# Kernel optimization log

Measured on AMD Instinct MI355X. Metric: run time of the kernel, lower is better.

Reference implementation:

```python
import jax, jax.numpy as jnp
import numpy as np
from jax.ops import segment_sum

N = 50000        # nodes
E = 800000       # edges
IN = 128         # in_channels
HID = 128        # hidden_channels
G = 256          # number of graphs


def setup_inputs() -> dict:
    key = jax.random.key(0)
    ks = jax.random.split(key, 24)

    def w(k, shape, fan_in):
        return (jax.random.normal(k, shape, dtype=jnp.float32) / np.sqrt(fan_in)).astype(jnp.float32)

    x = jax.random.normal(ks[0], (N, IN), dtype=jnp.float32)
    pos = jax.random.normal(ks[1], (N, 3), dtype=jnp.float32)
    edge_index = jax.random.randint(ks[2], (2, E), 0, N, dtype=jnp.int64)
    batch = jnp.sort(jax.random.randint(ks[3], (N,), 0, G, dtype=jnp.int64))

    params = dict(
        gcn_w=w(ks[4], (IN, HID), IN), gcn_b=jnp.zeros((HID,), jnp.float32),
        pam_w=w(ks[5], (IN, HID), IN), pam_b=jnp.zeros((HID,), jnp.float32),
        pm_w1=w(ks[6], (3, HID), 3), pm_b1=jnp.zeros((HID,), jnp.float32),
        pm_w2=w(ks[7], (HID, HID), HID), pm_b2=jnp.zeros((HID,), jnp.float32),
        att_w=w(ks[8], (2 * HID, 1), 2 * HID), att_b=jnp.zeros((1,), jnp.float32),
        fus_w=w(ks[9], (2 * HID, HID), 2 * HID), fus_b=jnp.zeros((HID,), jnp.float32),
        l1_w=w(ks[10], (HID, HID // 2), HID), l1_b=jnp.zeros((HID // 2,), jnp.float32),
        l2_w=w(ks[11], (HID // 2, 1), HID // 2), l2_b=jnp.zeros((1,), jnp.float32),
    )
    return dict(x=x, pos=pos, edge_index=edge_index, batch=batch, **params)


def reference(x, pos, edge_index, batch,
              gcn_w, gcn_b, pam_w, pam_b,
              pm_w1, pm_b1, pm_w2, pm_b2,
              att_w, att_b, fus_w, fus_b,
              l1_w, l1_b, l2_w, l2_b):
    n = x.shape[0]
    src, dst = edge_index[0], edge_index[1]  # j = source, i = target (PyG flow)

    # ---- global branch: GCNConv (self-loops + symmetric normalization) ----
    xw = x @ gcn_w                                   # [N, HID]
    loop = jnp.arange(n, dtype=src.dtype)
    s = jnp.concatenate([src, loop])
    d = jnp.concatenate([dst, loop])
    deg = segment_sum(jnp.ones_like(d, dtype=xw.dtype), d, num_segments=n)
    dinv = jnp.where(deg > 0, deg ** -0.5, 0.0)
    norm = dinv[s] * dinv[d]                          # [E+N]
    gcn = segment_sum(norm[:, None] * xw[s], d, num_segments=n) + gcn_b
    global_feat = jax.nn.relu(gcn)

    # ---- local branch: PAMConv ----
    xl = x @ pam_w + pam_b                            # [N, HID]
    x_i, x_j = xl[dst], xl[src]                       # [E, HID]
    delta = pos[dst] - pos[src]                       # [E, 3]
    de = jax.nn.relu(delta @ pm_w1 + pm_b1) @ pm_w2 + pm_b2   # [E, HID]
    att = jax.nn.sigmoid(jnp.concatenate([x_i, x_j], axis=-1) @ att_w + att_b)  # [E,1]
    msg = att * (x_j + de)
    local_feat = jax.nn.relu(segment_sum(msg, dst, num_segments=n))

    # ---- fusion + global mean pool + readout ----
    fused = jax.nn.relu(jnp.concatenate([global_feat, local_feat], axis=-1) @ fus_w + fus_b)
    counts = segment_sum(jnp.ones((n,), fused.dtype), batch, num_segments=G)
    pooled = segment_sum(fused, batch, num_segments=G) / jnp.clip(counts, 1.0)[:, None]
    h = jax.nn.relu(pooled @ l1_w + l1_b)
    return h @ l2_w + l2_b                            # [G, 1]
```

## Files before the change

kernel.cpp:

```cpp
#include <hip/hip_runtime.h>
#include <hip/hip_fp16.h>
#include <math.h>

#define NN 50000
#define NE 800000
#define HD 128
#define NG 256
#define SCAN_B 196
#define NODE_B 12500
#define HIST_B 3125
#define GEM_B 782
#define ZQ2 8192
#define WP_HIST0 73

typedef unsigned int u32;
typedef unsigned short u16;
typedef __attribute__((ext_vector_type(8))) short bf16x8;
typedef __attribute__((ext_vector_type(4))) float f32x4;
typedef __attribute__((ext_vector_type(2))) float f32x2;

__device__ __forceinline__ float wave_allsum(float v) {
#pragma unroll
  for (int m = 1; m < 64; m <<= 1) v += __shfl_xor(v, m, 64);
  return v;
}
__device__ __forceinline__ float bcastf(float v, int t) {
  return __int_as_float(__builtin_amdgcn_readlane(__float_as_int(v), t));
}
__device__ __forceinline__ u32 f2b_bits(float f) {
  u32 u = __float_as_uint(f);
  return (u + 0x7fffu + ((u >> 16) & 1u)) >> 16;
}
__device__ __forceinline__ u32 cvtpk_bf16(float lo, float hi) {
  u32 r;
  asm("v_cvt_pk_bf16_f32 %0, %1, %2" : "=v"(r) : "v"(lo), "v"(hi));
  return r;
}
__device__ __forceinline__ f32x2 splat2(float v) { return (f32x2){v, v}; }
__device__ __forceinline__ f32x2 pkfma(f32x2 a, f32x2 b, f32x2 c) {
  return a * b + c;
}

__global__ __launch_bounds__(256) void k_wpack(
    const float* __restrict__ gcn_w, const float* __restrict__ pam_w,
    const float* __restrict__ pm_w2, const float* __restrict__ fus_w,
    const float* __restrict__ pam_b, const float* __restrict__ att_w,
    const float* __restrict__ att_b, const float* __restrict__ pm_b2,
    u16* __restrict__ Bg, u16* __restrict__ Bl, u16* __restrict__ Bf,
    float* __restrict__ vi, float* __restrict__ vj,
    float* __restrict__ consts, float* __restrict__ bsumv,
    uint4* __restrict__ zr2, const int* __restrict__ ei,
    int* __restrict__ cnt, u16* __restrict__ slot16) {
  if (blockIdx.x >= WP_HIST0) {
    const int e = (blockIdx.x - WP_HIST0) * 256 + threadIdx.x;
    if (e < NE) slot16[e] = (u16)atomicAdd(&cnt[ei[NE + e]], 1);
    return;
  }
  if (blockIdx.x >= 41) {
    const int zi = (blockIdx.x - 41) * 256 + threadIdx.x;
    if (zi < ZQ2) zr2[zi] = (uint4){0u, 0u, 0u, 0u};
    return;
  }
  if (blockIdx.x == 40) {
    const int t = threadIdx.x;
    const int k = t & 127;
    const float* w = att_w + (t >> 7) * HD;
    float s = 0.f;
    for (int h = 0; h < HD; ++h) s = fmaf(pam_w[k * HD + h], w[h], s);
    if (t < 128) {
      vi[k] = s;
      bsumv[k] = pam_b[k] + pm_b2[k];
    } else {
      vj[k] = s;
    }
    if (t < 64) {
      float p = fmaf(pam_b[t], att_w[t], pam_b[t + 64] * att_w[t + 64]);
      p = wave_allsum(p);
      if (t == 0) consts[0] = p + att_b[0];
    } else if (t < 128) {
      const int l = t - 64;
      float p =
          fmaf(pam_b[l], att_w[HD + l], pam_b[l + 64] * att_w[HD + 64 + l]);
      p = wave_allsum(p);
      if (l == 0) consts[1] = p;
    }
    return;
  }
  const int t = blockIdx.x * 256 + threadIdx.x;
  const float* W;
  u16* dst;
  if (t < 2048) {
    const int kb = t >> 7, n = t & 127;
    W = gcn_w + (size_t)kb * 8 * HD + n;
    dst = Bg + (size_t)t * 8;
  } else if (t < 6144) {
    const int u = t - 2048;
    const int kb = u >> 7, n = u & 127;
    W = ((kb < 16) ? (pam_w + (size_t)kb * 8 * HD)
                   : (pm_w2 + (size_t)(kb - 16) * 8 * HD)) +
        n;
    dst = Bl + (size_t)u * 8;
  } else {
    const int u = t - 6144;
    const int kb = u >> 7, n = u & 127;
    W = fus_w + (size_t)kb * 8 * HD + n;
    dst = Bf + (size_t)u * 8;
  }
  union {
    u16 o[8];
    uint4 v;
  } pk;
#pragma unroll
  for (int i = 0; i < 8; ++i) pk.o[i] = (u16)f2b_bits(W[i * HD]);
  *(uint4*)dst = pk.v;
}

__global__ __launch_bounds__(256) void k_scan1(const int* __restrict__ cnt,
                                               int* __restrict__ bsum) {
  const int i = blockIdx.x * 256 + threadIdx.x;
  int v = (i < NN) ? cnt[i] : 0;
#pragma unroll
  for (int m = 1; m < 64; m <<= 1) v += __shfl_xor(v, m, 64);
  __shared__ int s[4];
  if ((threadIdx.x & 63) == 0) s[threadIdx.x >> 6] = v;
  __syncthreads();
  if (threadIdx.x == 0) bsum[blockIdx.x] = s[0] + s[1] + s[2] + s[3];
}

__global__ __launch_bounds__(256) void k_scan23(
    const int* __restrict__ cnt, const int* __restrict__ bsum,
    const float* __restrict__ pos, int* __restrict__ offs,
    float* __restrict__ dinv, float4* __restrict__ posadj) {
  __shared__ int s[256];
  const int t = threadIdx.x;
  const int bv = (t < SCAN_B) ? bsum[t] : 0;
  s[t] = bv;
  __syncthreads();
  for (int d = 1; d < 256; d <<= 1) {
    int add = (t >= d) ? s[t - d] : 0;
    __syncthreads();
    s[t] += add;
    __syncthreads();
  }
  const int bpre = (blockIdx.x > 0) ? s[blockIdx.x - 1] : 0;
  __syncthreads();
  const int i = blockIdx.x * 256 + t;
  const int v = (i < NN) ? cnt[i] : 0;
  s[t] = v;
  __syncthreads();
  for (int d = 1; d < 256; d <<= 1) {
    int add = (t >= d) ? s[t - d] : 0;
    __syncthreads();
    s[t] += add;
    __syncthreads();
  }
  if (i < NN) {
    offs[i] = bpre + s[t] - v;
    dinv[i] = __builtin_amdgcn_rsqf((float)v + 1.0f);
    posadj[i] = make_float4(pos[3 * i], pos[3 * i + 1], pos[3 * i + 2], 0.f);
  }
}

__global__ __launch_bounds__(256) void k_scatgc(
    const int* __restrict__ ei, const int* __restrict__ offs,
    const u16* __restrict__ slot16, int* __restrict__ csr_src,
    const int* __restrict__ batch, float* __restrict__ counts,
    const float* __restrict__ x, const float* __restrict__ dinv,
    const int* __restrict__ cnt, const float* __restrict__ vi,
    const float* __restrict__ vj, const float* __restrict__ consts,
    u16* __restrict__ xq, float* __restrict__ ai_arr,
    float4* __restrict__ posadj) {
  if (blockIdx.x < HIST_B) {
    const int e = blockIdx.x * 256 + threadIdx.x;
    if (e < NE) {
      const int d = ei[NE + e];
      csr_src[offs[d] + slot16[e]] = ei[e];
    }
    return;
  }
  if (blockIdx.x == HIST_B) {
    const int g = threadIdx.x;
    int lo = 0, hi = NN;
    while (lo < hi) {
      const int mid = (lo + hi) >> 1;
      if (batch[mid] < g) lo = mid + 1; else hi = mid;
    }
    const int b0 = lo;
    hi = NN;
    while (lo < hi) {
      const int mid = (lo + hi) >> 1;
      if (batch[mid] <= g) lo = mid + 1; else hi = mid;
    }
    counts[g] = (float)(lo - b0);
    return;
  }
  const int wave = threadIdx.x >> 6, lane = threadIdx.x & 63;
  const int i = (blockIdx.x - HIST_B - 1) * 4 + wave;
  if (i >= NN) return;
  const float2 v = *(const float2*)&x[(size_t)i * HD + lane * 2];
  const float dv = dinv[i];
  const u32 q = __builtin_amdgcn_cvt_pk_fp8_f32(dv * v.x, dv * v.y, 0u, false);
  xq[(size_t)i * 64 + lane] = (u16)q;
  const float2 a = *(const float2*)&vi[lane * 2];
  const float2 b = *(const float2*)&vj[lane * 2];
  float si = wave_allsum(fmaf(v.x, a.x, v.y * a.y));
  float sj = wave_allsum(fmaf(v.x, b.x, v.y * b.y));
  if (lane == 0) {
    ai_arr[i] = si + consts[0];
    const u32 wb =
        (u32)__half_as_ushort(__float2half(sj + consts[1])) |
        ((u32)__half_as_ushort(__float2half(sqrtf((float)cnt[i] + 1.f)))
         << 16);
    ((float*)(posadj + i))[3] = __uint_as_float(wb);
  }
}

__global__ __launch_bounds__(256) void k_agg(
    const u16* __restrict__ xq, const float4* __restrict__ posadj,
    const int* __restrict__ csr_src, const int* __restrict__ offs,
    const int* __restrict__ cnt, const float* __restrict__ ai_arr,
    const float* __restrict__ pm_w1, const float* __restrict__ pm_b1,
    u32* __restrict__ ZG, u32* __restrict__ XT, float* __restrict__ sa_out) {
  const int wave = threadIdx.x >> 6, lane = threadIdx.x & 63;
  const int i = blockIdx.x * 4 + wave;
  if (i >= NN) return;
  const int c0 = lane * 2;

  const f32x2 w1x = *(const f32x2*)&pm_w1[c0];
  const f32x2 w1y = *(const f32x2*)&pm_w1[HD + c0];
  const f32x2 w1z = *(const f32x2*)&pm_w1[2 * HD + c0];
  const f32x2 b1 = *(const f32x2*)&pm_b1[c0];
  const float ai = ai_arr[i];
  const float4 pi = posadj[i];

  f32x2 zg = {0.f, 0.f}, xa = {0.f, 0.f}, tt = {0.f, 0.f};
  float sa = 0.f;
  const int b = offs[i], e = b + cnt[i];
  for (int base = b; base < e; base += 64) {
    const int mm = min(64, e - base);
    const int sk = csr_src[base + ((lane < mm) ? lane : 0)];
    const float4 pa = posadj[sk];
    const u32 wb = __float_as_uint(pa.w);
    const float aj = __half2float(__ushort_as_half((u16)(wb & 0xffffu)));
    const float sdeg = __half2float(__ushort_as_half((u16)(wb >> 16)));
    float attk = __builtin_amdgcn_rcpf(1.f + __expf(-(ai + aj)));
    const float apk = attk * sdeg;
    const float dxk = pi.x - pa.x;
    const float dyk = pi.y - pa.y;
    const float dzk = pi.z - pa.z;
    if (lane >= mm) attk = 0.f;
    sa += wave_allsum(attk);

    for (int s16 = 0; s16 < mm; s16 += 16) {
      const int n16 = min(16, mm - s16);
      u32 rr[16];
#pragma unroll
      for (int u = 0; u < 16; ++u) {
        if (u < n16) {
          const int s = __builtin_amdgcn_readlane(sk, s16 + u);
          rr[u] = *(xq + ((size_t)s << 6) + lane);
        }
      }
#pragma unroll
      for (int u = 0; u < 16; ++u) {
        if (u < n16) {
          const int T = s16 + u;
          const float att = bcastf(attk, T);
          const float ap = bcastf(apk, T);
          const float dx = bcastf(dxk, T);
          const float dy = bcastf(dyk, T);
          const float dz = bcastf(dzk, T);
          const f32x2 y = __builtin_amdgcn_cvt_pk_f32_fp8(rr[u], false);
          zg += y;
          xa = pkfma(splat2(ap), y, xa);
          f32x2 gg = pkfma(splat2(dz), w1z,
                           pkfma(splat2(dy), w1y,
                                 pkfma(splat2(dx), w1x, b1)));
          gg = __builtin_elementwise_max(gg, splat2(0.f));
          tt = pkfma(splat2(att), gg, tt);
        }
      }
    }
  }
  const u32 xi = *(xq + ((size_t)i << 6) + lane);
  zg += __builtin_amdgcn_cvt_pk_f32_fp8(xi, false);

  ZG[(size_t)i * 64 + lane] = cvtpk_bf16(zg.x, zg.y);
  XT[(size_t)i * 128 + lane] = cvtpk_bf16(xa.x, xa.y);
  XT[(size_t)i * 128 + 64 + lane] = cvtpk_bf16(tt.x, tt.y);
  if (lane == 0) sa_out[i] = sa;
}

template <int K16>
__device__ __forceinline__ void phase_g2(const u16* __restrict__ pa,
                                         const u16* __restrict__ pb0,
                                         f32x4 acc[8]) {
  bf16x8 a[3], b[3][8];
#pragma unroll
  for (int p = 0; p < 2; ++p) {
    a[p] = *(const bf16x8*)(pa + p * 32);
    const u16* pn = pb0 + (size_t)p * 4096;
#pragma unroll
    for (int cf = 0; cf < 8; ++cf) b[p][cf] = *(const bf16x8*)(pn + cf * 128);
  }
#pragma unroll
  for (int k0 = 0; k0 < K16; ++k0) {
    if (k0 + 2 < K16) {
      const int nb = (k0 + 2) % 3;
      a[nb] = *(const bf16x8*)(pa + (k0 + 2) * 32);
      const u16* pn = pb0 + (size_t)(k0 + 2) * 4096;
#pragma unroll
      for (int cf = 0; cf < 8; ++cf)
        b[nb][cf] = *(const bf16x8*)(pn + cf * 128);
    }
    const int cb = k0 % 3;
#pragma unroll
    for (int cf = 0; cf < 8; ++cf)
      acc[cf] = __builtin_amdgcn_mfma_f32_16x16x32_bf16(a[cb], b[cb][cf],
                                                        acc[cf], 0, 0, 0);
  }
}

__global__ __launch_bounds__(256, 3) void k_gemms(
    const u16* __restrict__ ZG, const u16* __restrict__ XT,
    const u16* __restrict__ Bg, const u16* __restrict__ Bl,
    const u16* __restrict__ Bf, const float* __restrict__ dinv,
    const float* __restrict__ sa, const float* __restrict__ gcn_b,
    const float* __restrict__ bsumv, const float* __restrict__ fus_b,
    const int* __restrict__ batch, float* __restrict__ pooled) {
  __shared__ u16 T[64 * 256];
  __shared__ int batch_lds[64];
  const int n0 = blockIdx.x * 64;
  const int t = threadIdx.x, lane = t & 63, w = t >> 6;
  const int m = lane & 15, g = lane >> 4;
  const int r0 = w * 16;

  if (t < 64) batch_lds[t] = (n0 + t < NN) ? batch[n0 + t] : -1;

  const int rowA = min(n0 + r0 + m, NN - 1);
  f32x4 acc[8];

#pragma unroll
  for (int cf = 0; cf < 8; ++cf) acc[cf] = (f32x4){0.f, 0.f, 0.f, 0.f};
  phase_g2<4>(ZG + (size_t)rowA * 128 + g * 8, Bg + ((size_t)g * HD + m) * 8,
              acc);
#pragma unroll
  for (int j = 0; j < 4; ++j) {
    const int rl = r0 + g * 4 + j;
    const float dv = dinv[min(n0 + rl, NN - 1)];
#pragma unroll
    for (int cf = 0; cf < 8; ++cf) {
      const float v = fmaxf(fmaf(dv, acc[cf][j], gcn_b[cf * 16 + m]), 0.f);
      T[rl * 256 + ((cf * 16 + m) ^ ((rl & 7) << 3))] = (u16)f2b_bits(v);
    }
  }

#pragma unroll
  for (int cf = 0; cf < 8; ++cf) acc[cf] = (f32x4){0.f, 0.f, 0.f, 0.f};
  phase_g2<8>(XT + (size_t)rowA * 256 + g * 8, Bl + ((size_t)g * HD + m) * 8,
              acc);
#pragma unroll
  for (int j = 0; j < 4; ++j) {
    const int rl = r0 + g * 4 + j;
    const float sv = sa[min(n0 + rl, NN - 1)];
#pragma unroll
    for (int cf = 0; cf < 8; ++cf) {
      const float v = fmaxf(fmaf(sv, bsumv[cf * 16 + m], acc[cf][j]), 0.f);
      T[rl * 256 + ((128 + cf * 16 + m) ^ ((rl & 7) << 3))] = (u16)f2b_bits(v);
    }
  }

  const int x0m = (m & 7) << 3;
  const u16* rowT = &T[(r0 + m) * 256];
  const u16* pbC = Bf + ((size_t)g * HD + m) * 8;
#pragma unroll
  for (int cf = 0; cf < 8; ++cf) acc[cf] = (f32x4){0.f, 0.f, 0.f, 0.f};
  {
    bf16x8 a[3], b[3][8];
#pragma unroll
    for (int p = 0; p < 2; ++p) {
      a[p] = *(const bf16x8*)&rowT[(g * 8 + p * 32) ^ x0m];
      const u16* pn = pbC + (size_t)p * 4096;
#pragma unroll
      for (int cf = 0; cf < 8; ++cf) b[p][cf] = *(const bf16x8*)(pn + cf * 128);
    }
#pragma unroll
    for (int k0 = 0; k0 < 8; ++k0) {
      if (k0 + 2 < 8) {
        const int nb = (k0 + 2) % 3;
        a[nb] = *(const bf16x8*)&rowT[(g * 8 + (k0 + 2) * 32) ^ x0m];
        const u16* pn = pbC + (size_t)(k0 + 2) * 4096;
#pragma unroll
        for (int cf = 0; cf < 8; ++cf)
          b[nb][cf] = *(const bf16x8*)(pn + cf * 128);
      }
      const int cb = k0 % 3;
#pragma unroll
      for (int cf = 0; cf < 8; ++cf)
        acc[cf] = __builtin_amdgcn_mfma_f32_16x16x32_bf16(a[cb], b[cb][cf],
                                                          acc[cf], 0, 0, 0);
    }
  }
  float* F = (float*)T;
#pragma unroll
  for (int j = 0; j < 4; ++j) {
    const int rl = r0 + g * 4 + j;
#pragma unroll
    for (int cf = 0; cf < 8; ++cf)
      F[rl * 128 + ((cf * 16 + m) ^ ((rl & 12) << 2))] =
          fmaxf(acc[cf][j] + fus_b[cf * 16 + m], 0.f);
  }
  __syncthreads();

  const int col = t & 127;
  const int q = t >> 7;
  int seg = -1;
  float run = 0.f;
  for (int r = q * 32; r < q * 32 + 32; ++r) {
    const int bg = batch_lds[r];
    const float v = F[r * 128 + (col ^ ((r & 12) << 2))];
    if (bg != seg) {
      if (seg >= 0) atomicAdd(&pooled[seg * HD + col], run);
      seg = bg;
      run = 0.f;
    }
    if (bg >= 0) run += v;
  }
  if (seg >= 0) atomicAdd(&pooled[seg * HD + col], run);
}

__global__ __launch_bounds__(64) void k_head(const float* __restrict__ pooled,
                                             const float* __restrict__ counts,
                                             const float* __restrict__ l1w,
                                             const float* __restrict__ l1b,
                                             const float* __restrict__ l2w,
                                             const float* __restrict__ l2b,
                                             float* __restrict__ out) {
  const int g = blockIdx.x, j = threadIdx.x;
  const float inv = __builtin_amdgcn_rcpf(fmaxf(counts[g], 1.f));
  float acc = l1b[j];
  for (int k = 0; k < HD; ++k)
    acc = fmaf(pooled[g * HD + k] * inv, l1w[k * 64 + j], acc);
  float v = fmaxf(acc, 0.f) * l2w[j];
  v = wave_allsum(v);
  if (j == 0) out[g] = v + l2b[0];
}

extern "C" void kernel_launch(void* const* d_in, const int* in_sizes, int n_in,
                              void* d_out, int out_size, void* d_ws,
                              size_t ws_size, hipStream_t stream) {
  const float* x = (const float*)d_in[0];
  const float* pos = (const float*)d_in[1];
  const int* ei = (const int*)d_in[2];
  const int* batch = (const int*)d_in[3];
  const float* gcn_w = (const float*)d_in[4];
  const float* gcn_b = (const float*)d_in[5];
  const float* pam_w = (const float*)d_in[6];
  const float* pam_b = (const float*)d_in[7];
  const float* pm_w1 = (const float*)d_in[8];
  const float* pm_b1 = (const float*)d_in[9];
  const float* pm_w2 = (const float*)d_in[10];
  const float* pm_b2 = (const float*)d_in[11];
  const float* att_w = (const float*)d_in[12];
  const float* att_b = (const float*)d_in[13];
  const float* fus_w = (const float*)d_in[14];
  const float* fus_b = (const float*)d_in[15];
  const float* l1_w = (const float*)d_in[16];
  const float* l1_b = (const float*)d_in[17];
  const float* l2_w = (const float*)d_in[18];
  const float* l2_b = (const float*)d_in[19];
  float* out = (float*)d_out;

  size_t off = 0;
  auto alloc = [&](size_t bytes) {
    void* p = (char*)d_ws + off;
    off += (bytes + 255) & ~size_t(255);
    return p;
  };
  u16* xq = (u16*)alloc((size_t)NN * 64 * 2);
  u32* ZG = (u32*)alloc((size_t)NN * 64 * 4);
  u32* XT = (u32*)alloc((size_t)NN * 128 * 4);
  float* sa = (float*)alloc((size_t)NN * 4);
  float* ai = (float*)alloc((size_t)NN * 4);
  float* dinv = (float*)alloc((size_t)NN * 4);
  float4* posadj = (float4*)alloc((size_t)NN * 16);
  float* pooled = (float*)alloc((size_t)NG * HD * 4);
  float* counts = (float*)alloc((size_t)NG * 4);
  int* cnt = (int*)alloc((size_t)NN * 4);
  int* offs = (int*)alloc((size_t)NN * 4);
  int* csr_src = (int*)alloc((size_t)NE * 4);
  u16* slot16 = (u16*)alloc((size_t)NE * 2);
  int* bsum = (int*)alloc((size_t)SCAN_B * 4);
  u16* Bg = (u16*)alloc((size_t)16 * 128 * 8 * 2);
  u16* Bl = (u16*)alloc((size_t)32 * 128 * 8 * 2);
  u16* Bf = (u16*)alloc((size_t)32 * 128 * 8 * 2);
  float* vi = (float*)alloc(128 * 4);
  float* vj = (float*)alloc(128 * 4);
  float* consts = (float*)alloc(2 * 4);
  float* bsumv = (float*)alloc(128 * 4);

  hipMemsetAsync(cnt, 0, NN * 4, stream);
  k_wpack<<<WP_HIST0 + HIST_B, 256, 0, stream>>>(
      gcn_w, pam_w, pm_w2, fus_w, pam_b, att_w, att_b, pm_b2, Bg, Bl, Bf, vi,
      vj, consts, bsumv, (uint4*)pooled, ei, cnt, slot16);
  k_scan1<<<SCAN_B, 256, 0, stream>>>(cnt, bsum);
  k_scan23<<<SCAN_B, 256, 0, stream>>>(cnt, bsum, pos, offs, dinv, posadj);
  k_scatgc<<<HIST_B + 1 + NODE_B, 256, 0, stream>>>(
      ei, offs, slot16, csr_src, batch, counts, x, dinv, cnt, vi, vj, consts,
      xq, ai, posadj);
  k_agg<<<NODE_B, 256, 0, stream>>>(xq, posadj, csr_src, offs, cnt, ai, pm_w1,
                                    pm_b1, ZG, XT, sa);
  k_gemms<<<GEM_B, 256, 0, stream>>>((const u16*)ZG, (const u16*)XT, Bg, Bl,
                                     Bf, dinv, sa, gcn_b, bsumv, fus_b, batch,
                                     pooled);
  k_head<<<NG, 64, 0, stream>>>(pooled, counts, l1_w, l1_b, l2_w, l2_b, out);
}
```

Measured before the change: 159.6 us.

## Store CSR sources as 16-bit indices and move node prep into scan kernel

The CSR source array is narrowed from 32-bit to 16-bit indices, relying on the node count fitting in u16. This halves the bytes moved by the edge scatter and by the neighbor-index reads in the aggregation kernel. The per-node fp8 quantization, attention dot products and posadj packing move from the scatter kernel into extra blocks of the scan kernel. There dinv is recomputed from cnt and posadj is written once as a full float4 instead of in two partial writes. The risk is that the index encoding silently breaks if the node count exceeds 65535.

Result: slower. 163.1 us (+2.2%).

```diff
diff --git a/kernel.cpp b/kernel.cpp
--- a/kernel.cpp
+++ b/kernel.cpp
@@ -129,8 +129,35 @@
 
 __global__ __launch_bounds__(256) void k_scan23(
     const int* __restrict__ cnt, const int* __restrict__ bsum,
-    const float* __restrict__ pos, int* __restrict__ offs,
-    float* __restrict__ dinv, float4* __restrict__ posadj) {
+    const float* __restrict__ pos, const float* __restrict__ x,
+    const float* __restrict__ vi, const float* __restrict__ vj,
+    const float* __restrict__ consts, int* __restrict__ offs,
+    float* __restrict__ dinv, float4* __restrict__ posadj,
+    u16* __restrict__ xq, float* __restrict__ ai_arr) {
+  if (blockIdx.x >= SCAN_B) {
+    const int wave = threadIdx.x >> 6, lane = threadIdx.x & 63;
+    const int i = (blockIdx.x - SCAN_B) * 4 + wave;
+    if (i >= NN) return;
+    const float2 v = *(const float2*)&x[(size_t)i * HD + lane * 2];
+    const int c = cnt[i];
+    const float dv = __builtin_amdgcn_rsqf((float)c + 1.0f);
+    const u32 q =
+        __builtin_amdgcn_cvt_pk_fp8_f32(dv * v.x, dv * v.y, 0u, false);
+    xq[(size_t)i * 64 + lane] = (u16)q;
+    const float2 a = *(const float2*)&vi[lane * 2];
+    const float2 b = *(const float2*)&vj[lane * 2];
+    float si = wave_allsum(fmaf(v.x, a.x, v.y * a.y));
+    float sj = wave_allsum(fmaf(v.x, b.x, v.y * b.y));
+    if (lane == 0) {
+      ai_arr[i] = si + consts[0];
+      const u32 wb =
+          (u32)__half_as_ushort(__float2half(sj + consts[1])) |
+          ((u32)__half_as_ushort(__float2half(sqrtf((float)c + 1.f))) << 16);
+      posadj[i] = make_float4(pos[3 * i], pos[3 * i + 1], pos[3 * i + 2],
+                              __uint_as_float(wb));
+    }
+    return;
+  }
   __shared__ int s[256];
   const int t = threadIdx.x;
   const int bv = (t < SCAN_B) ? bsum[t] : 0;
@@ -157,67 +184,39 @@
   if (i < NN) {
     offs[i] = bpre + s[t] - v;
     dinv[i] = __builtin_amdgcn_rsqf((float)v + 1.0f);
-    posadj[i] = make_float4(pos[3 * i], pos[3 * i + 1], pos[3 * i + 2], 0.f);
   }
 }
 
 __global__ __launch_bounds__(256) void k_scatgc(
     const int* __restrict__ ei, const int* __restrict__ offs,
-    const u16* __restrict__ slot16, int* __restrict__ csr_src,
-    const int* __restrict__ batch, float* __restrict__ counts,
-    const float* __restrict__ x, const float* __restrict__ dinv,
-    const int* __restrict__ cnt, const float* __restrict__ vi,
-    const float* __restrict__ vj, const float* __restrict__ consts,
-    u16* __restrict__ xq, float* __restrict__ ai_arr,
-    float4* __restrict__ posadj) {
+    const u16* __restrict__ slot16, u16* __restrict__ csr16,
+    const int* __restrict__ batch, float* __restrict__ counts) {
   if (blockIdx.x < HIST_B) {
     const int e = blockIdx.x * 256 + threadIdx.x;
     if (e < NE) {
       const int d = ei[NE + e];
-      csr_src[offs[d] + slot16[e]] = ei[e];
+      csr16[offs[d] + slot16[e]] = (u16)ei[e];
     }
     return;
   }
-  if (blockIdx.x == HIST_B) {
-    const int g = threadIdx.x;
-    int lo = 0, hi = NN;
-    while (lo < hi) {
-      const int mid = (lo + hi) >> 1;
-      if (batch[mid] < g) lo = mid + 1; else hi = mid;
-    }
-    const int b0 = lo;
-    hi = NN;
-    while (lo < hi) {
-      const int mid = (lo + hi) >> 1;
-      if (batch[mid] <= g) lo = mid + 1; else hi = mid;
-    }
-    counts[g] = (float)(lo - b0);
-    return;
-  }
-  const int wave = threadIdx.x >> 6, lane = threadIdx.x & 63;
-  const int i = (blockIdx.x - HIST_B - 1) * 4 + wave;
-  if (i >= NN) return;
-  const float2 v = *(const float2*)&x[(size_t)i * HD + lane * 2];
-  const float dv = dinv[i];
-  const u32 q = __builtin_amdgcn_cvt_pk_fp8_f32(dv * v.x, dv * v.y, 0u, false);
-  xq[(size_t)i * 64 + lane] = (u16)q;
-  const float2 a = *(const float2*)&vi[lane * 2];
-  const float2 b = *(const float2*)&vj[lane * 2];
-  float si = wave_allsum(fmaf(v.x, a.x, v.y * a.y));
-  float sj = wave_allsum(fmaf(v.x, b.x, v.y * b.y));
-  if (lane == 0) {
-    ai_arr[i] = si + consts[0];
-    const u32 wb =
-        (u32)__half_as_ushort(__float2half(sj + consts[1])) |
-        ((u32)__half_as_ushort(__float2half(sqrtf((float)cnt[i] + 1.f)))
-         << 16);
-    ((float*)(posadj + i))[3] = __uint_as_float(wb);
-  }
+  const int g = threadIdx.x;
+  int lo = 0, hi = NN;
+  while (lo < hi) {
+    const int mid = (lo + hi) >> 1;
+    if (batch[mid] < g) lo = mid + 1; else hi = mid;
+  }
+  const int b0 = lo;
+  hi = NN;
+  while (lo < hi) {
+    const int mid = (lo + hi) >> 1;
+    if (batch[mid] <= g) lo = mid + 1; else hi = mid;
+  }
+  counts[g] = (float)(lo - b0);
 }
 
 __global__ __launch_bounds__(256) void k_agg(
     const u16* __restrict__ xq, const float4* __restrict__ posadj,
-    const int* __restrict__ csr_src, const int* __restrict__ offs,
+    const u16* __restrict__ csr16, const int* __restrict__ offs,
     const int* __restrict__ cnt, const float* __restrict__ ai_arr,
     const float* __restrict__ pm_w1, const float* __restrict__ pm_b1,
     u32* __restrict__ ZG, u32* __restrict__ XT, float* __restrict__ sa_out) {
@@ -238,7 +237,7 @@
   const int b = offs[i], e = b + cnt[i];
   for (int base = b; base < e; base += 64) {
     const int mm = min(64, e - base);
-    const int sk = csr_src[base + ((lane < mm) ? lane : 0)];
+    const int sk = (int)csr16[base + ((lane < mm) ? lane : 0)];
     const float4 pa = posadj[sk];
     const u32 wb = __float_as_uint(pa.w);
     const float aj = __half2float(__ushort_as_half((u16)(wb & 0xffffu)));
@@ -488,7 +487,7 @@
   float* counts = (float*)alloc((size_t)NG * 4);
   int* cnt = (int*)alloc((size_t)NN * 4);
   int* offs = (int*)alloc((size_t)NN * 4);
-  int* csr_src = (int*)alloc((size_t)NE * 4);
+  u16* csr16 = (u16*)alloc((size_t)NE * 2);
   u16* slot16 = (u16*)alloc((size_t)NE * 2);
   int* bsum = (int*)alloc((size_t)SCAN_B * 4);
   u16* Bg = (u16*)alloc((size_t)16 * 128 * 8 * 2);
@@ -504,11 +503,12 @@
       gcn_w, pam_w, pm_w2, fus_w, pam_b, att_w, att_b, pm_b2, Bg, Bl, Bf, vi,
       vj, consts, bsumv, (uint4*)pooled, ei, cnt, slot16);
   k_scan1<<<SCAN_B, 256, 0, stream>>>(cnt, bsum);
-  k_scan23<<<SCAN_B, 256, 0, stream>>>(cnt, bsum, pos, offs, dinv, posadj);
-  k_scatgc<<<HIST_B + 1 + NODE_B, 256, 0, stream>>>(
-      ei, offs, slot16, csr_src, batch, counts, x, dinv, cnt, vi, vj, consts,
-      xq, ai, posadj);
-  k_agg<<<NODE_B, 256, 0, stream>>>(xq, posadj, csr_src, offs, cnt, ai, pm_w1,
+  k_scan23<<<SCAN_B + NODE_B, 256, 0, stream>>>(cnt, bsum, pos, x, vi, vj,
+                                                consts, offs, dinv, posadj,
+                                                xq, ai);
+  k_scatgc<<<HIST_B + 1, 256, 0, stream>>>(ei, offs, slot16, csr16, batch,
+                                           counts);
+  k_agg<<<NODE_B, 256, 0, stream>>>(xq, posadj, csr16, offs, cnt, ai, pm_w1,
                                     pm_b1, ZG, XT, sa);
   k_gemms<<<GEM_B, 256, 0, stream>>>((const u16*)ZG, (const u16*)XT, Bg, Bl,
                                      Bf, dinv, sa, gcn_b, bsumv, fus_b, batch,
```
